# Optimization experiments

Measured on AMD Instinct MI355X. Metric: run time of the kernel, lower is better.

## Reference

```python
import jax, jax.numpy as jnp
import numpy as np

B, HH, WW, C = 2, 128, 128, 256
HEADS, KA, DR = 8, 3, 4
D = C // DR // HEADS          # 8 per-head channels
KK = KA * KA                  # 9 neighborhood positions
ATTN_DIM = KK * HEADS         # 72
DIMS = (ATTN_DIM // 4, ATTN_DIM // 2, ATTN_DIM)  # gnConv dims [18,36,72] (order=3)
SD = sum(DIMS)                # 126
S = 1.0                       # self.scale = s in __init__ (overrides qk scale)


def conv2d(x, w, b, pad, groups=1):
    out = jax.lax.conv_general_dilated(
        x, w, (1, 1), [(pad, pad), (pad, pad)],
        dimension_numbers=("NCHW", "OIHW", "NCHW"), feature_group_count=groups)
    return out + b[None, :, None, None]


def setup_inputs() -> dict:
    key = jax.random.key(0)
    ks = jax.random.split(key, 16)
    def rn(i, shape, s=0.02):
        return jax.random.normal(ks[i], shape, dtype=jnp.float32) * s
    return {
        "x": jax.random.normal(ks[0], (B, HH * WW, C), dtype=jnp.float32),
        "qkv_w": rn(1, (C, 3 * C // DR)),
        "qkv_b": jnp.zeros((3 * C // DR,), jnp.float32),
        "dc1_dw_w": rn(2, (D, 1, KA, KA)),
        "dc1_dw_b": jnp.zeros((D,), jnp.float32),
        "dc1_pw_w": rn(3, (KK * D, D, 3, 3)),
        "dc1_pw_b": jnp.zeros((KK * D,), jnp.float32),
        "dc2_dw_w": rn(4, (D, 1, KA, KA)),
        "dc2_dw_b": jnp.zeros((D,), jnp.float32),
        "dc2_pw_w": rn(5, (KK * D, D, 3, 3)),
        "dc2_pw_b": jnp.zeros((KK * D,), jnp.float32),
        "rpb": rn(6, (1, HEADS, 1, KK, 1, 1)),
        "pin_w": rn(7, (2 * ATTN_DIM, ATTN_DIM, 1, 1)),
        "pin_b": jnp.zeros((2 * ATTN_DIM,), jnp.float32),
        "dw7_w": rn(8, (SD, 1, 7, 7)),
        "dw7_b": jnp.zeros((SD,), jnp.float32),
        "dw5_w": rn(9, (SD, 1, 5, 5)),
        "dw5_b": jnp.zeros((SD,), jnp.float32),
        "dw3_w": rn(10, (SD, 1, 3, 3)),
        "dw3_b": jnp.zeros((SD,), jnp.float32),
        "pw1_w": rn(11, (DIMS[1], DIMS[0], 1, 1)),
        "pw1_b": jnp.zeros((DIMS[1],), jnp.float32),
        "pw2_w": rn(12, (DIMS[2], DIMS[1], 1, 1)),
        "pw2_b": jnp.zeros((DIMS[2],), jnp.float32),
        "pout_w": rn(13, (ATTN_DIM, ATTN_DIM, 1, 1)),
        "pout_b": jnp.zeros((ATTN_DIM,), jnp.float32),
        "proj_w": rn(14, (C // DR, C)),
        "proj_b": jnp.zeros((C,), jnp.float32),
        "H": HH,
        "W": WW,
    }


def reference(x, qkv_w, qkv_b, dc1_dw_w, dc1_dw_b, dc1_pw_w, dc1_pw_b,
              dc2_dw_w, dc2_dw_b, dc2_pw_w, dc2_pw_b, rpb, pin_w, pin_b,
              dw7_w, dw7_b, dw5_w, dw5_b, dw3_w, dw3_b,
              pw1_w, pw1_b, pw2_w, pw2_b, pout_w, pout_b, proj_w, proj_b, H, W):
    Bx, N, Cx = x.shape
    xi = x.reshape(Bx, H, W, Cx)
    qkv = xi @ qkv_w + qkv_b                                   # (B,H,W,3C/DR)
    f = jnp.transpose(qkv, (0, 3, 1, 2)).reshape(Bx * HEADS, 3 * D, H, W)
    q = (f[:, :D] * S).reshape(Bx, HEADS, D, 1, H, W)
    k_in = f[:, D:2 * D]                                       # (B*heads, D, H, W)
    v_in = f[:, 2 * D:]

    def dep(y):  # shared dep_conv + dep_conv1: KAxKA depthwise then 3x3 D->KK*D expand
        a = conv2d(conv2d(y, dc1_dw_w, dc1_dw_b, KA // 2, groups=D), dc1_pw_w, dc1_pw_b, 1)
        b2 = conv2d(conv2d(y, dc2_dw_w, dc2_dw_b, KA // 2, groups=D), dc2_pw_w, dc2_pw_b, 1)
        return (a + b2).reshape(Bx, HEADS, D, KK, H, W)

    k = dep(k_in) + rpb                                        # relative position bias
    v = dep(v_in)
    attn1 = jax.nn.softmax((q * k).sum(2, keepdims=True), axis=3)  # (B,heads,1,KK,H,W)

    # gnConv (recursive gated conv) on attention maps
    attn = attn1.reshape(Bx, HEADS * KK, H, W)                 # (B,72,H,W)
    fused = conv2d(attn, pin_w, pin_b, 0)                      # (B,144,H,W)
    pwa, abc = fused[:, :DIMS[0]], fused[:, DIMS[0]:]          # 18 / 126
    dw = conv2d(abc, dw7_w, dw7_b, 3, groups=SD)
    dw = conv2d(jax.nn.relu(dw), dw5_w, dw5_b, 2, groups=SD)
    dw = conv2d(jax.nn.relu(dw), dw3_w, dw3_b, 1, groups=SD) * S
    d0 = dw[:, :DIMS[0]]
    d1 = dw[:, DIMS[0]:DIMS[0] + DIMS[1]]
    d2 = dw[:, DIMS[0] + DIMS[1]:]
    g = pwa * d0
    g = conv2d(g, pw1_w, pw1_b, 0) * d1
    g = conv2d(g, pw2_w, pw2_b, 0) * d2
    g = conv2d(g, pout_w, pout_b, 0).reshape(Bx, HEADS, 1, KK, H, W)

    out = ((g * v) + (attn1 * v)).sum(3).reshape(Bx, Cx // DR, H, W)
    out = jnp.transpose(out, (0, 2, 3, 1)) @ proj_w + proj_b   # Linear C/DR -> C
    return out.reshape(Bx, N, Cx)
```

## Files before the change

### kernel.cpp

```cpp
#include <hip/hip_runtime.h>

#define IH 128
#define IW 128
#define NPI (IH*IW)

__global__ __launch_bounds__(256) void k_wt(const float* __restrict__ w1,
                                            const float* __restrict__ w2,
                                            float* __restrict__ wT) {
  int i = blockIdx.x * 256 + threadIdx.x;
  if (i < 72 * 72) {
    int c = i / 72, dkk = i % 72;
    wT[dkk * 144 + c]      = w1[i];
    wT[dkk * 144 + 72 + c] = w2[i];
  }
}

__global__ __launch_bounds__(256) void k_qkv(const float* __restrict__ x,
                                             const float* __restrict__ w,
                                             const float* __restrict__ bias,
                                             float* __restrict__ f) {
  int t = threadIdx.x;
  int lane = t & 63;
  int wv = __builtin_amdgcn_readfirstlane(t >> 6);
  int gp = blockIdx.x * 64 + lane;
  int b = gp >> 14;
  int pp = gp & (NPI - 1);
  const float* xrow = x + (size_t)gp * 256;
  int jbase = wv * 48;
  float acc[48];
#pragma unroll
  for (int jj = 0; jj < 48; ++jj) acc[jj] = bias[jbase + jj];
  for (int c = 0; c < 256; c += 8) {
    float xr[8];
#pragma unroll
    for (int q4 = 0; q4 < 2; ++q4) {
      float4 v = *reinterpret_cast<const float4*>(xrow + c + q4 * 4);
      xr[q4 * 4 + 0] = v.x; xr[q4 * 4 + 1] = v.y;
      xr[q4 * 4 + 2] = v.z; xr[q4 * 4 + 3] = v.w;
    }
#pragma unroll
    for (int jt = 0; jt < 48; jt += 4) {
#pragma unroll
      for (int cc = 0; cc < 8; ++cc) {
        const float* wp = w + (c + cc) * 192 + jbase + jt;
        acc[jt + 0] += xr[cc] * wp[0];
        acc[jt + 1] += xr[cc] * wp[1];
        acc[jt + 2] += xr[cc] * wp[2];
        acc[jt + 3] += xr[cc] * wp[3];
      }
    }
  }
#pragma unroll
  for (int jj = 0; jj < 48; ++jj) {
    int j = jbase + jj;
    f[((size_t)(b * 192 + j)) * NPI + pp] = acc[jj];
  }
}

template <int MODE>
__global__ __launch_bounds__(256) void k_dep(const float* __restrict__ f,
    const float* __restrict__ dwW1, const float* __restrict__ dwB1,
    const float* __restrict__ dwW2, const float* __restrict__ dwB2,
    const float* __restrict__ wT,  const float* __restrict__ pwB1,
    const float* __restrict__ pwB2, const float* __restrict__ rpb,
    const float* __restrict__ gout, const float* __restrict__ attn_in,
    float* __restrict__ outp) {
  __shared__ float kin[8][20][20];
  __shared__ float dwa[8][18][18];
  __shared__ float dwb[8][18][18];
  int t = threadIdx.x;
  int tile = blockIdx.x;
  int bh = blockIdx.y;
  int h = bh & 7;
  int y0 = (tile >> 3) << 4, x0 = (tile & 7) << 4;
  const float* src = f + ((size_t)(bh * 24 + (MODE ? 16 : 8))) * NPI;
  for (int idx = t; idx < 8 * 20 * 20; idx += 256) {
    int c = idx / 400, r = idx % 400, yy = r / 20, xx = r % 20;
    int ay = y0 - 2 + yy, ax = x0 - 2 + xx;
    float v = 0.f;
    if ((unsigned)ay < (unsigned)IH && (unsigned)ax < (unsigned)IW)
      v = src[c * NPI + ay * IW + ax];
    kin[c][yy][xx] = v;
  }
  __syncthreads();
  for (int idx = t; idx < 8 * 18 * 18; idx += 256) {
    int c = idx / 324, r = idx % 324, yy = r / 18, xx = r % 18;
    int ay = y0 - 1 + yy, ax = x0 - 1 + xx;
    float va = 0.f, vb = 0.f;
    if ((unsigned)ay < (unsigned)IH && (unsigned)ax < (unsigned)IW) {
      va = dwB1[c]; vb = dwB2[c];
#pragma unroll
      for (int ky = 0; ky < 3; ++ky)
#pragma unroll
        for (int kx = 0; kx < 3; ++kx) {
          float s = kin[c][yy + ky][xx + kx];
          va += dwW1[c * 9 + ky * 3 + kx] * s;
          vb += dwW2[c * 9 + ky * 3 + kx] * s;
        }
    }
    dwa[c][yy][xx] = va;
    dwb[c][yy][xx] = vb;
  }
  __syncthreads();
  int ly = t >> 4, lx = t & 15;
  int p = (y0 + ly) * IW + (x0 + lx);
  float acc[72];
#pragma unroll
  for (int c = 0; c < 72; ++c) {
    acc[c] = pwB1[c] + pwB2[c];
    if (MODE == 0) acc[c] += rpb[h * 9 + (c % 9)];
  }
#pragma unroll 1
  for (int dkk = 0; dkk < 72; ++dkk) {
    int d = dkk / 9; int t9 = dkk - d * 9; int ky = t9 / 3; int kx = t9 - ky * 3;
    float v1 = dwa[d][ly + ky][lx + kx];
    float v2 = dwb[d][ly + ky][lx + kx];
    const float* wp = wT + dkk * 144;
#pragma unroll
    for (int c = 0; c < 72; ++c) {
      acc[c] += wp[c] * v1;
      acc[c] += wp[72 + c] * v2;
    }
  }
  if (MODE == 0) {
    float q[8];
#pragma unroll
    for (int d = 0; d < 8; ++d) q[d] = f[((size_t)(bh * 24 + d)) * NPI + p];
    float e[9];
    float m = -1e30f;
#pragma unroll
    for (int kk = 0; kk < 9; ++kk) {
      float s = 0.f;
#pragma unroll
      for (int d = 0; d < 8; ++d) s += q[d] * acc[d * 9 + kk];
      e[kk] = s;
      m = fmaxf(m, s);
    }
    float sum = 0.f;
#pragma unroll
    for (int kk = 0; kk < 9; ++kk) { e[kk] = __expf(e[kk] - m); sum += e[kk]; }
    float r = 1.f / sum;
#pragma unroll
    for (int kk = 0; kk < 9; ++kk)
      outp[((size_t)(bh * 9 + kk)) * NPI + p] = e[kk] * r;
  } else {
    float coef[9];
#pragma unroll
    for (int kk = 0; kk < 9; ++kk)
      coef[kk] = gout[((size_t)(bh * 9 + kk)) * NPI + p] +
                 attn_in[((size_t)(bh * 9 + kk)) * NPI + p];
#pragma unroll
    for (int d = 0; d < 8; ++d) {
      float s = 0.f;
#pragma unroll
      for (int kk = 0; kk < 9; ++kk) s += coef[kk] * acc[d * 9 + kk];
      outp[((size_t)(bh * 8 + d)) * NPI + p] = s;
    }
  }
}

__global__ __launch_bounds__(256) void k_pin(const float* __restrict__ attn,
                                             const float* __restrict__ w,
                                             const float* __restrict__ bias,
                                             float* __restrict__ fused) {
  int t = threadIdx.x, lane = t & 63;
  int wv = __builtin_amdgcn_readfirstlane(t >> 6);
  int gp = blockIdx.x * 64 + lane;
  int b = gp >> 14, p = gp & (NPI - 1);
  const float* ap = attn + (size_t)b * 72 * NPI + p;
  float a[72];
#pragma unroll
  for (int i = 0; i < 72; ++i) a[i] = ap[i * NPI];
  int j0 = wv * 36;
#pragma unroll 1
  for (int jj = 0; jj < 36; ++jj) {
    int j = j0 + jj;
    const float* wp = w + j * 72;
    float s = bias[j];
#pragma unroll
    for (int i = 0; i < 72; ++i) s += wp[i] * a[i];
    fused[((size_t)b * 144 + j) * NPI + p] = s;
  }
}

__global__ __launch_bounds__(256) void k_dwchain(const float* __restrict__ fused,
    const float* __restrict__ w7, const float* __restrict__ b7,
    const float* __restrict__ w5, const float* __restrict__ b5,
    const float* __restrict__ w3, const float* __restrict__ b3,
    float* __restrict__ dwout) {
  __shared__ float s_in[28][28];
  __shared__ float s_t7[22][22];
  __shared__ float s_t5[18][18];
  int t = threadIdx.x;
  int tile = blockIdx.x;
  int c = blockIdx.y;
  int b = blockIdx.z;
  int y0 = (tile >> 3) << 4, x0 = (tile & 7) << 4;
  const float* src = fused + ((size_t)b * 144 + 18 + c) * NPI;
  for (int idx = t; idx < 28 * 28; idx += 256) {
    int yy = idx / 28, xx = idx % 28;
    int ay = y0 - 6 + yy, ax = x0 - 6 + xx;
    s_in[yy][xx] = ((unsigned)ay < (unsigned)IH && (unsigned)ax < (unsigned)IW)
                       ? src[ay * IW + ax] : 0.f;
  }
  __syncthreads();
  for (int idx = t; idx < 22 * 22; idx += 256) {
    int yy = idx / 22, xx = idx % 22;
    int ay = y0 - 3 + yy, ax = x0 - 3 + xx;
    float s = 0.f;
    if ((unsigned)ay < (unsigned)IH && (unsigned)ax < (unsigned)IW) {
      s = b7[c];
#pragma unroll
      for (int ky = 0; ky < 7; ++ky)
#pragma unroll
        for (int kx = 0; kx < 7; ++kx)
          s += w7[c * 49 + ky * 7 + kx] * s_in[yy + ky][xx + kx];
      s = fmaxf(s, 0.f);
    }
    s_t7[yy][xx] = s;
  }
  __syncthreads();
  for (int idx = t; idx < 18 * 18; idx += 256) {
    int yy = idx / 18, xx = idx % 18;
    int ay = y0 - 1 + yy, ax = x0 - 1 + xx;
    float s = 0.f;
    if ((unsigned)ay < (unsigned)IH && (unsigned)ax < (unsigned)IW) {
      s = b5[c];
#pragma unroll
      for (int ky = 0; ky < 5; ++ky)
#pragma unroll
        for (int kx = 0; kx < 5; ++kx)
          s += w5[c * 25 + ky * 5 + kx] * s_t7[yy + ky][xx + kx];
      s = fmaxf(s, 0.f);
    }
    s_t5[yy][xx] = s;
  }
  __syncthreads();
  int ly = t >> 4, lx = t & 15;
  float s = b3[c];
#pragma unroll
  for (int ky = 0; ky < 3; ++ky)
#pragma unroll
    for (int kx = 0; kx < 3; ++kx)
      s += w3[c * 9 + ky * 3 + kx] * s_t5[ly + ky][lx + kx];
  dwout[((size_t)b * 126 + c) * NPI + (y0 + ly) * IW + (x0 + lx)] = s;
}

__global__ __launch_bounds__(256) void k_g1(const float* __restrict__ fused,
                                            const float* __restrict__ dw,
                                            const float* __restrict__ w,
                                            const float* __restrict__ bias,
                                            float* __restrict__ g2) {
  int t = threadIdx.x, lane = t & 63;
  int wv = __builtin_amdgcn_readfirstlane(t >> 6);
  int gp = blockIdx.x * 64 + lane;
  int b = gp >> 14, p = gp & (NPI - 1);
  const float* fu = fused + (size_t)b * 144 * NPI + p;
  const float* dp = dw + (size_t)b * 126 * NPI + p;
  float g1v[18];
#pragma unroll
  for (int i = 0; i < 18; ++i) g1v[i] = fu[i * NPI] * dp[i * NPI];
  int j0 = wv * 9;
#pragma unroll 1
  for (int jj = 0; jj < 9; ++jj) {
    int j = j0 + jj;
    const float* wp = w + j * 18;
    float s = bias[j];
#pragma unroll
    for (int i = 0; i < 18; ++i) s += wp[i] * g1v[i];
    s *= dp[(18 + j) * NPI];
    g2[((size_t)b * 36 + j) * NPI + p] = s;
  }
}

__global__ __launch_bounds__(256) void k_g2(const float* __restrict__ g2in,
                                            const float* __restrict__ dw,
                                            const float* __restrict__ w,
                                            const float* __restrict__ bias,
                                            float* __restrict__ g3) {
  int t = threadIdx.x, lane = t & 63;
  int wv = __builtin_amdgcn_readfirstlane(t >> 6);
  int gp = blockIdx.x * 64 + lane;
  int b = gp >> 14, p = gp & (NPI - 1);
  const float* ip = g2in + (size_t)b * 36 * NPI + p;
  const float* dp = dw + (size_t)b * 126 * NPI + p;
  float g[36];
#pragma unroll
  for (int i = 0; i < 36; ++i) g[i] = ip[i * NPI];
  int j0 = wv * 18;
#pragma unroll 1
  for (int jj = 0; jj < 18; ++jj) {
    int j = j0 + jj;
    const float* wp = w + j * 36;
    float s = bias[j];
#pragma unroll
    for (int i = 0; i < 36; ++i) s += wp[i] * g[i];
    s *= dp[(54 + j) * NPI];
    g3[((size_t)b * 72 + j) * NPI + p] = s;
  }
}

__global__ __launch_bounds__(256) void k_g3(const float* __restrict__ g3in,
                                            const float* __restrict__ w,
                                            const float* __restrict__ bias,
                                            float* __restrict__ gout) {
  int t = threadIdx.x, lane = t & 63;
  int wv = __builtin_amdgcn_readfirstlane(t >> 6);
  int gp = blockIdx.x * 64 + lane;
  int b = gp >> 14, p = gp & (NPI - 1);
  const float* ip = g3in + (size_t)b * 72 * NPI + p;
  float g[72];
#pragma unroll
  for (int i = 0; i < 72; ++i) g[i] = ip[i * NPI];
  int j0 = wv * 18;
#pragma unroll 1
  for (int jj = 0; jj < 18; ++jj) {
    int j = j0 + jj;
    const float* wp = w + j * 72;
    float s = bias[j];
#pragma unroll
    for (int i = 0; i < 72; ++i) s += wp[i] * g[i];
    gout[((size_t)b * 72 + j) * NPI + p] = s;
  }
}

__global__ __launch_bounds__(256) void k_proj(const float* __restrict__ pre,
                                              const float* __restrict__ w,
                                              const float* __restrict__ bias,
                                              float* __restrict__ out) {
  int t = threadIdx.x;
  int blk = blockIdx.x;
  int b = (blk * 64) >> 14;
  int p0 = (blk * 64) & (NPI - 1);
  const float* pp = pre + (size_t)b * 64 * NPI + p0;
  float wreg[64];
#pragma unroll
  for (int i = 0; i < 64; ++i) wreg[i] = w[i * 256 + t];
  float bs = bias[t];
#pragma unroll 1
  for (int px = 0; px < 64; ++px) {
    float s = bs;
#pragma unroll
    for (int i = 0; i < 64; ++i) s += wreg[i] * pp[i * NPI + px];
    out[((size_t)(b * NPI + p0 + px)) * 256 + t] = s;
  }
}

extern "C" void kernel_launch(void* const* d_in, const int* in_sizes, int n_in,
                              void* d_out, int out_size, void* d_ws, size_t ws_size,
                              hipStream_t stream) {
  const float* x        = (const float*)d_in[0];
  const float* qkv_w    = (const float*)d_in[1];
  const float* qkv_b    = (const float*)d_in[2];
  const float* dc1_dw_w = (const float*)d_in[3];
  const float* dc1_dw_b = (const float*)d_in[4];
  const float* dc1_pw_w = (const float*)d_in[5];
  const float* dc1_pw_b = (const float*)d_in[6];
  const float* dc2_dw_w = (const float*)d_in[7];
  const float* dc2_dw_b = (const float*)d_in[8];
  const float* dc2_pw_w = (const float*)d_in[9];
  const float* dc2_pw_b = (const float*)d_in[10];
  const float* rpb      = (const float*)d_in[11];
  const float* pin_w    = (const float*)d_in[12];
  const float* pin_b    = (const float*)d_in[13];
  const float* dw7_w    = (const float*)d_in[14];
  const float* dw7_b    = (const float*)d_in[15];
  const float* dw5_w    = (const float*)d_in[16];
  const float* dw5_b    = (const float*)d_in[17];
  const float* dw3_w    = (const float*)d_in[18];
  const float* dw3_b    = (const float*)d_in[19];
  const float* pw1_w    = (const float*)d_in[20];
  const float* pw1_b    = (const float*)d_in[21];
  const float* pw2_w    = (const float*)d_in[22];
  const float* pw2_b    = (const float*)d_in[23];
  const float* pout_w   = (const float*)d_in[24];
  const float* pout_b   = (const float*)d_in[25];
  const float* proj_w   = (const float*)d_in[26];
  const float* proj_b   = (const float*)d_in[27];
  (void)in_sizes; (void)n_in; (void)out_size; (void)ws_size;

  float* fbuf = (float*)d_out;
  float* ws    = (float*)d_ws;
  float* wT    = ws;
  float* attn1 = wT + 10368;
  float* fused = attn1 + 2359296;
  float* dwout = fused + 4718592;
  float* g2b   = dwout + 4128768;
  float* g3b   = g2b + 1179648;
  float* goutb = g3b + 2359296;
  float* pre   = goutb + 2359296;

  hipLaunchKernelGGL(k_wt, dim3(21), dim3(256), 0, stream, dc1_pw_w, dc2_pw_w, wT);
  hipLaunchKernelGGL(k_qkv, dim3(512), dim3(256), 0, stream, x, qkv_w, qkv_b, fbuf);
  hipLaunchKernelGGL((k_dep<0>), dim3(64, 16), dim3(256), 0, stream, fbuf,
                     dc1_dw_w, dc1_dw_b, dc2_dw_w, dc2_dw_b, wT, dc1_pw_b, dc2_pw_b,
                     rpb, (const float*)nullptr, (const float*)nullptr, attn1);
  hipLaunchKernelGGL(k_pin, dim3(512), dim3(256), 0, stream, attn1, pin_w, pin_b, fused);
  hipLaunchKernelGGL(k_dwchain, dim3(64, 126, 2), dim3(256), 0, stream, fused,
                     dw7_w, dw7_b, dw5_w, dw5_b, dw3_w, dw3_b, dwout);
  hipLaunchKernelGGL(k_g1, dim3(512), dim3(256), 0, stream, fused, dwout, pw1_w, pw1_b, g2b);
  hipLaunchKernelGGL(k_g2, dim3(512), dim3(256), 0, stream, g2b, dwout, pw2_w, pw2_b, g3b);
  hipLaunchKernelGGL(k_g3, dim3(512), dim3(256), 0, stream, g3b, pout_w, pout_b, goutb);
  hipLaunchKernelGGL((k_dep<1>), dim3(64, 16), dim3(256), 0, stream, fbuf,
                     dc1_dw_w, dc1_dw_b, dc2_dw_w, dc2_dw_b, wT, dc1_pw_b, dc2_pw_b,
                     rpb, goutb, attn1, pre);
  hipLaunchKernelGGL(k_proj, dim3(512), dim3(256), 0, stream, pre, proj_w, proj_b,
                     (float*)d_out);
}
```

Measured before the change: 566.1 us.

## Fuse gnConv pointwise chain, stage qkv input in LDS, enlarge dwchain tiles

Merges the three gnConv pointwise kernels into one that keeps the 36- and 72-channel intermediates in shared memory, which removes two global round trips and two launches. The qkv kernel now stages the 64-pixel input tile in padded LDS so loads are coalesced. The depthwise chain uses 32x32 tiles to cut halo recompute. Other changes add launch_bounds occupancy hints, explicit FMAs, padded dep shared arrays, hoisted q/coef loads, and 4-pixel blocking in proj. The risks are register pressure from the occupancy hints and larger LDS footprints that may lower occupancy.

```diff
diff --git a/kernel.cpp b/kernel.cpp
--- a/kernel.cpp
+++ b/kernel.cpp
@@ -15,50 +15,50 @@
   }
 }
 
-__global__ __launch_bounds__(256) void k_qkv(const float* __restrict__ x,
-                                             const float* __restrict__ w,
-                                             const float* __restrict__ bias,
-                                             float* __restrict__ f) {
+__global__ __launch_bounds__(256, 4) void k_qkv(const float* __restrict__ x,
+                                                const float* __restrict__ w,
+                                                const float* __restrict__ bias,
+                                                float* __restrict__ f) {
+  __shared__ float xs[64][257];
   int t = threadIdx.x;
   int lane = t & 63;
-  int wv = __builtin_amdgcn_readfirstlane(t >> 6);
-  int gp = blockIdx.x * 64 + lane;
-  int b = gp >> 14;
-  int pp = gp & (NPI - 1);
-  const float* xrow = x + (size_t)gp * 256;
+  int wv = t >> 6;
+  int p0 = blockIdx.x * 64;
+  int b = p0 >> 14;
+  int pp = p0 & (NPI - 1);
+#pragma unroll
+  for (int k = 0; k < 16; ++k) {
+    int vi = k * 256 + t;
+    int px = vi >> 6;
+    int c = (vi & 63) * 4;
+    float4 v = *reinterpret_cast<const float4*>(x + (size_t)(p0 + px) * 256 + c);
+    xs[px][c] = v.x; xs[px][c + 1] = v.y; xs[px][c + 2] = v.z; xs[px][c + 3] = v.w;
+  }
+  __syncthreads();
   int jbase = wv * 48;
   float acc[48];
 #pragma unroll
   for (int jj = 0; jj < 48; ++jj) acc[jj] = bias[jbase + jj];
+#pragma unroll 1
   for (int c = 0; c < 256; c += 8) {
     float xr[8];
 #pragma unroll
-    for (int q4 = 0; q4 < 2; ++q4) {
-      float4 v = *reinterpret_cast<const float4*>(xrow + c + q4 * 4);
-      xr[q4 * 4 + 0] = v.x; xr[q4 * 4 + 1] = v.y;
-      xr[q4 * 4 + 2] = v.z; xr[q4 * 4 + 3] = v.w;
-    }
-#pragma unroll
-    for (int jt = 0; jt < 48; jt += 4) {
-#pragma unroll
-      for (int cc = 0; cc < 8; ++cc) {
-        const float* wp = w + (c + cc) * 192 + jbase + jt;
-        acc[jt + 0] += xr[cc] * wp[0];
-        acc[jt + 1] += xr[cc] * wp[1];
-        acc[jt + 2] += xr[cc] * wp[2];
-        acc[jt + 3] += xr[cc] * wp[3];
-      }
-    }
-  }
-#pragma unroll
-  for (int jj = 0; jj < 48; ++jj) {
-    int j = jbase + jj;
-    f[((size_t)(b * 192 + j)) * NPI + pp] = acc[jj];
-  }
+    for (int cc = 0; cc < 8; ++cc) xr[cc] = xs[lane][c + cc];
+#pragma unroll
+    for (int cc = 0; cc < 8; ++cc) {
+      const float* wp = w + (size_t)(c + cc) * 192 + jbase;
+#pragma unroll
+      for (int jj = 0; jj < 48; ++jj)
+        acc[jj] = __builtin_fmaf(xr[cc], wp[jj], acc[jj]);
+    }
+  }
+#pragma unroll
+  for (int jj = 0; jj < 48; ++jj)
+    f[((size_t)(b * 192 + jbase + jj)) * NPI + pp + lane] = acc[jj];
 }
 
 template <int MODE>
-__global__ __launch_bounds__(256) void k_dep(const float* __restrict__ f,
+__global__ __launch_bounds__(256, 4) void k_dep(const float* __restrict__ f,
     const float* __restrict__ dwW1, const float* __restrict__ dwB1,
     const float* __restrict__ dwW2, const float* __restrict__ dwB2,
     const float* __restrict__ wT,  const float* __restrict__ pwB1,
@@ -66,8 +66,8 @@
     const float* __restrict__ gout, const float* __restrict__ attn_in,
     float* __restrict__ outp) {
   __shared__ float kin[8][20][20];
-  __shared__ float dwa[8][18][18];
-  __shared__ float dwb[8][18][18];
+  __shared__ float dwa[8][18][20];
+  __shared__ float dwb[8][18][20];
   int t = threadIdx.x;
   int tile = blockIdx.x;
   int bh = blockIdx.y;
@@ -94,8 +94,8 @@
 #pragma unroll
         for (int kx = 0; kx < 3; ++kx) {
           float s = kin[c][yy + ky][xx + kx];
-          va += dwW1[c * 9 + ky * 3 + kx] * s;
-          vb += dwW2[c * 9 + ky * 3 + kx] * s;
+          va = __builtin_fmaf(dwW1[c * 9 + ky * 3 + kx], s, va);
+          vb = __builtin_fmaf(dwW2[c * 9 + ky * 3 + kx], s, vb);
         }
     }
     dwa[c][yy][xx] = va;
@@ -110,29 +110,39 @@
     acc[c] = pwB1[c] + pwB2[c];
     if (MODE == 0) acc[c] += rpb[h * 9 + (c % 9)];
   }
+  float q[8]; float coef[9];
+  if (MODE == 0) {
+#pragma unroll
+    for (int d = 0; d < 8; ++d) q[d] = f[((size_t)(bh * 24 + d)) * NPI + p];
+  } else {
+#pragma unroll
+    for (int kk = 0; kk < 9; ++kk)
+      coef[kk] = gout[((size_t)(bh * 9 + kk)) * NPI + p] +
+                 attn_in[((size_t)(bh * 9 + kk)) * NPI + p];
+  }
 #pragma unroll 1
-  for (int dkk = 0; dkk < 72; ++dkk) {
-    int d = dkk / 9; int t9 = dkk - d * 9; int ky = t9 / 3; int kx = t9 - ky * 3;
-    float v1 = dwa[d][ly + ky][lx + kx];
-    float v2 = dwb[d][ly + ky][lx + kx];
-    const float* wp = wT + dkk * 144;
-#pragma unroll
-    for (int c = 0; c < 72; ++c) {
-      acc[c] += wp[c] * v1;
-      acc[c] += wp[72 + c] * v2;
+  for (int d = 0; d < 8; ++d) {
+#pragma unroll
+    for (int t9 = 0; t9 < 9; ++t9) {
+      const int ky = t9 / 3, kx = t9 % 3;
+      const float v1 = dwa[d][ly + ky][lx + kx];
+      const float v2 = dwb[d][ly + ky][lx + kx];
+      const float* wp = wT + (size_t)(d * 9 + t9) * 144;
+#pragma unroll
+      for (int c = 0; c < 72; ++c) {
+        acc[c] = __builtin_fmaf(wp[c], v1, acc[c]);
+        acc[c] = __builtin_fmaf(wp[72 + c], v2, acc[c]);
+      }
     }
   }
   if (MODE == 0) {
-    float q[8];
-#pragma unroll
-    for (int d = 0; d < 8; ++d) q[d] = f[((size_t)(bh * 24 + d)) * NPI + p];
     float e[9];
     float m = -1e30f;
 #pragma unroll
     for (int kk = 0; kk < 9; ++kk) {
       float s = 0.f;
 #pragma unroll
-      for (int d = 0; d < 8; ++d) s += q[d] * acc[d * 9 + kk];
+      for (int d = 0; d < 8; ++d) s = __builtin_fmaf(q[d], acc[d * 9 + kk], s);
       e[kk] = s;
       m = fmaxf(m, s);
     }
@@ -144,27 +154,22 @@
     for (int kk = 0; kk < 9; ++kk)
       outp[((size_t)(bh * 9 + kk)) * NPI + p] = e[kk] * r;
   } else {
-    float coef[9];
-#pragma unroll
-    for (int kk = 0; kk < 9; ++kk)
-      coef[kk] = gout[((size_t)(bh * 9 + kk)) * NPI + p] +
-                 attn_in[((size_t)(bh * 9 + kk)) * NPI + p];
 #pragma unroll
     for (int d = 0; d < 8; ++d) {
       float s = 0.f;
 #pragma unroll
-      for (int kk = 0; kk < 9; ++kk) s += coef[kk] * acc[d * 9 + kk];
+      for (int kk = 0; kk < 9; ++kk) s = __builtin_fmaf(coef[kk], acc[d * 9 + kk], s);
       outp[((size_t)(bh * 8 + d)) * NPI + p] = s;
     }
   }
 }
 
-__global__ __launch_bounds__(256) void k_pin(const float* __restrict__ attn,
-                                             const float* __restrict__ w,
-                                             const float* __restrict__ bias,
-                                             float* __restrict__ fused) {
+__global__ __launch_bounds__(256, 4) void k_pin(const float* __restrict__ attn,
+                                                const float* __restrict__ w,
+                                                const float* __restrict__ bias,
+                                                float* __restrict__ fused) {
   int t = threadIdx.x, lane = t & 63;
-  int wv = __builtin_amdgcn_readfirstlane(t >> 6);
+  int wv = t >> 6;
   int gp = blockIdx.x * 64 + lane;
   int b = gp >> 14, p = gp & (NPI - 1);
   const float* ap = attn + (size_t)b * 72 * NPI + p;
@@ -172,40 +177,40 @@
 #pragma unroll
   for (int i = 0; i < 72; ++i) a[i] = ap[i * NPI];
   int j0 = wv * 36;
-#pragma unroll 1
+#pragma unroll 2
   for (int jj = 0; jj < 36; ++jj) {
     int j = j0 + jj;
     const float* wp = w + j * 72;
     float s = bias[j];
 #pragma unroll
-    for (int i = 0; i < 72; ++i) s += wp[i] * a[i];
+    for (int i = 0; i < 72; ++i) s = __builtin_fmaf(wp[i], a[i], s);
     fused[((size_t)b * 144 + j) * NPI + p] = s;
   }
 }
 
-__global__ __launch_bounds__(256) void k_dwchain(const float* __restrict__ fused,
+__global__ __launch_bounds__(256, 4) void k_dwchain(const float* __restrict__ fused,
     const float* __restrict__ w7, const float* __restrict__ b7,
     const float* __restrict__ w5, const float* __restrict__ b5,
     const float* __restrict__ w3, const float* __restrict__ b3,
     float* __restrict__ dwout) {
-  __shared__ float s_in[28][28];
-  __shared__ float s_t7[22][22];
-  __shared__ float s_t5[18][18];
+  __shared__ float s_in[44][44];
+  __shared__ float s_t7[38][38];
+  __shared__ float s_t5[34][34];
   int t = threadIdx.x;
   int tile = blockIdx.x;
   int c = blockIdx.y;
   int b = blockIdx.z;
-  int y0 = (tile >> 3) << 4, x0 = (tile & 7) << 4;
+  int y0 = (tile >> 2) << 5, x0 = (tile & 3) << 5;
   const float* src = fused + ((size_t)b * 144 + 18 + c) * NPI;
-  for (int idx = t; idx < 28 * 28; idx += 256) {
-    int yy = idx / 28, xx = idx % 28;
+  for (int idx = t; idx < 44 * 44; idx += 256) {
+    int yy = idx / 44, xx = idx % 44;
     int ay = y0 - 6 + yy, ax = x0 - 6 + xx;
     s_in[yy][xx] = ((unsigned)ay < (unsigned)IH && (unsigned)ax < (unsigned)IW)
                        ? src[ay * IW + ax] : 0.f;
   }
   __syncthreads();
-  for (int idx = t; idx < 22 * 22; idx += 256) {
-    int yy = idx / 22, xx = idx % 22;
+  for (int idx = t; idx < 38 * 38; idx += 256) {
+    int yy = idx / 38, xx = idx % 38;
     int ay = y0 - 3 + yy, ax = x0 - 3 + xx;
     float s = 0.f;
     if ((unsigned)ay < (unsigned)IH && (unsigned)ax < (unsigned)IW) {
@@ -214,14 +219,14 @@
       for (int ky = 0; ky < 7; ++ky)
 #pragma unroll
         for (int kx = 0; kx < 7; ++kx)
-          s += w7[c * 49 + ky * 7 + kx] * s_in[yy + ky][xx + kx];
+          s = __builtin_fmaf(w7[c * 49 + ky * 7 + kx], s_in[yy + ky][xx + kx], s);
       s = fmaxf(s, 0.f);
     }
     s_t7[yy][xx] = s;
   }
   __syncthreads();
-  for (int idx = t; idx < 18 * 18; idx += 256) {
-    int yy = idx / 18, xx = idx % 18;
+  for (int idx = t; idx < 34 * 34; idx += 256) {
+    int yy = idx / 34, xx = idx % 34;
     int ay = y0 - 1 + yy, ax = x0 - 1 + xx;
     float s = 0.f;
     if ((unsigned)ay < (unsigned)IH && (unsigned)ax < (unsigned)IW) {
@@ -230,29 +235,34 @@
       for (int ky = 0; ky < 5; ++ky)
 #pragma unroll
         for (int kx = 0; kx < 5; ++kx)
-          s += w5[c * 25 + ky * 5 + kx] * s_t7[yy + ky][xx + kx];
+          s = __builtin_fmaf(w5[c * 25 + ky * 5 + kx], s_t7[yy + ky][xx + kx], s);
       s = fmaxf(s, 0.f);
     }
     s_t5[yy][xx] = s;
   }
   __syncthreads();
-  int ly = t >> 4, lx = t & 15;
-  float s = b3[c];
-#pragma unroll
-  for (int ky = 0; ky < 3; ++ky)
-#pragma unroll
-    for (int kx = 0; kx < 3; ++kx)
-      s += w3[c * 9 + ky * 3 + kx] * s_t5[ly + ky][lx + kx];
-  dwout[((size_t)b * 126 + c) * NPI + (y0 + ly) * IW + (x0 + lx)] = s;
-}
-
-__global__ __launch_bounds__(256) void k_g1(const float* __restrict__ fused,
-                                            const float* __restrict__ dw,
-                                            const float* __restrict__ w,
-                                            const float* __restrict__ bias,
-                                            float* __restrict__ g2) {
+  for (int idx = t; idx < 32 * 32; idx += 256) {
+    int py = idx >> 5, px = idx & 31;
+    float s = b3[c];
+#pragma unroll
+    for (int ky = 0; ky < 3; ++ky)
+#pragma unroll
+      for (int kx = 0; kx < 3; ++kx)
+        s = __builtin_fmaf(w3[c * 9 + ky * 3 + kx], s_t5[py + ky][px + kx], s);
+    dwout[((size_t)b * 126 + c) * NPI + (y0 + py) * IW + (x0 + px)] = s;
+  }
+}
+
+__global__ __launch_bounds__(256, 4) void k_gchain(const float* __restrict__ fused,
+    const float* __restrict__ dw,
+    const float* __restrict__ pw1_w, const float* __restrict__ pw1_b,
+    const float* __restrict__ pw2_w, const float* __restrict__ pw2_b,
+    const float* __restrict__ pout_w, const float* __restrict__ pout_b,
+    float* __restrict__ gout) {
+  __shared__ float t36[36][64];
+  __shared__ float t72[72][64];
   int t = threadIdx.x, lane = t & 63;
-  int wv = __builtin_amdgcn_readfirstlane(t >> 6);
+  int wv = t >> 6;
   int gp = blockIdx.x * 64 + lane;
   int b = gp >> 14, p = gp & (NPI - 1);
   const float* fu = fused + (size_t)b * 144 * NPI + p;
@@ -260,74 +270,58 @@
   float g1v[18];
 #pragma unroll
   for (int i = 0; i < 18; ++i) g1v[i] = fu[i * NPI] * dp[i * NPI];
-  int j0 = wv * 9;
-#pragma unroll 1
-  for (int jj = 0; jj < 9; ++jj) {
-    int j = j0 + jj;
-    const float* wp = w + j * 18;
-    float s = bias[j];
-#pragma unroll
-    for (int i = 0; i < 18; ++i) s += wp[i] * g1v[i];
-    s *= dp[(18 + j) * NPI];
-    g2[((size_t)b * 36 + j) * NPI + p] = s;
-  }
-}
-
-__global__ __launch_bounds__(256) void k_g2(const float* __restrict__ g2in,
-                                            const float* __restrict__ dw,
-                                            const float* __restrict__ w,
-                                            const float* __restrict__ bias,
-                                            float* __restrict__ g3) {
-  int t = threadIdx.x, lane = t & 63;
-  int wv = __builtin_amdgcn_readfirstlane(t >> 6);
-  int gp = blockIdx.x * 64 + lane;
-  int b = gp >> 14, p = gp & (NPI - 1);
-  const float* ip = g2in + (size_t)b * 36 * NPI + p;
-  const float* dp = dw + (size_t)b * 126 * NPI + p;
-  float g[36];
-#pragma unroll
-  for (int i = 0; i < 36; ++i) g[i] = ip[i * NPI];
-  int j0 = wv * 18;
-#pragma unroll 1
-  for (int jj = 0; jj < 18; ++jj) {
-    int j = j0 + jj;
-    const float* wp = w + j * 36;
-    float s = bias[j];
-#pragma unroll
-    for (int i = 0; i < 36; ++i) s += wp[i] * g[i];
-    s *= dp[(54 + j) * NPI];
-    g3[((size_t)b * 72 + j) * NPI + p] = s;
-  }
-}
-
-__global__ __launch_bounds__(256) void k_g3(const float* __restrict__ g3in,
-                                            const float* __restrict__ w,
-                                            const float* __restrict__ bias,
-                                            float* __restrict__ gout) {
-  int t = threadIdx.x, lane = t & 63;
-  int wv = __builtin_amdgcn_readfirstlane(t >> 6);
-  int gp = blockIdx.x * 64 + lane;
-  int b = gp >> 14, p = gp & (NPI - 1);
-  const float* ip = g3in + (size_t)b * 72 * NPI + p;
-  float g[72];
-#pragma unroll
-  for (int i = 0; i < 72; ++i) g[i] = ip[i * NPI];
-  int j0 = wv * 18;
-#pragma unroll 1
-  for (int jj = 0; jj < 18; ++jj) {
-    int j = j0 + jj;
-    const float* wp = w + j * 72;
-    float s = bias[j];
-#pragma unroll
-    for (int i = 0; i < 72; ++i) s += wp[i] * g[i];
-    gout[((size_t)b * 72 + j) * NPI + p] = s;
-  }
-}
-
-__global__ __launch_bounds__(256) void k_proj(const float* __restrict__ pre,
-                                              const float* __restrict__ w,
-                                              const float* __restrict__ bias,
-                                              float* __restrict__ out) {
+  {
+    int j0 = wv * 9;
+#pragma unroll 2
+    for (int jj = 0; jj < 9; ++jj) {
+      int j = j0 + jj;
+      const float* wp = pw1_w + j * 18;
+      float s = pw1_b[j];
+#pragma unroll
+      for (int i = 0; i < 18; ++i) s = __builtin_fmaf(wp[i], g1v[i], s);
+      s *= dp[(18 + j) * NPI];
+      t36[j][lane] = s;
+    }
+  }
+  __syncthreads();
+  {
+    float a36[36];
+#pragma unroll
+    for (int i = 0; i < 36; ++i) a36[i] = t36[i][lane];
+    int j0 = wv * 18;
+#pragma unroll 2
+    for (int jj = 0; jj < 18; ++jj) {
+      int j = j0 + jj;
+      const float* wp = pw2_w + j * 36;
+      float s = pw2_b[j];
+#pragma unroll
+      for (int i = 0; i < 36; ++i) s = __builtin_fmaf(wp[i], a36[i], s);
+      s *= dp[(54 + j) * NPI];
+      t72[j][lane] = s;
+    }
+  }
+  __syncthreads();
+  {
+    float a72[72];
+#pragma unroll
+    for (int i = 0; i < 72; ++i) a72[i] = t72[i][lane];
+    int j0 = wv * 18;
+#pragma unroll 2
+    for (int jj = 0; jj < 18; ++jj) {
+      int j = j0 + jj;
+      const float* wp = pout_w + j * 72;
+      float s = pout_b[j];
+#pragma unroll
+      for (int i = 0; i < 72; ++i) s = __builtin_fmaf(wp[i], a72[i], s);
+      gout[((size_t)b * 72 + j) * NPI + p] = s;
+    }
+  }
+}
+
+__global__ __launch_bounds__(256, 4) void k_proj(const float* __restrict__ pre,
+                                                 const float* __restrict__ w,
+                                                 const float* __restrict__ bias,
+                                                 float* __restrict__ out) {
   int t = threadIdx.x;
   int blk = blockIdx.x;
   int b = (blk * 64) >> 14;
@@ -338,11 +332,18 @@
   for (int i = 0; i < 64; ++i) wreg[i] = w[i * 256 + t];
   float bs = bias[t];
 #pragma unroll 1
-  for (int px = 0; px < 64; ++px) {
-    float s = bs;
-#pragma unroll
-    for (int i = 0; i < 64; ++i) s += wreg[i] * pp[i * NPI + px];
-    out[((size_t)(b * NPI + p0 + px)) * 256 + t] = s;
+  for (int px4 = 0; px4 < 16; ++px4) {
+    float s0 = bs, s1 = bs, s2 = bs, s3 = bs;
+#pragma unroll
+    for (int i = 0; i < 64; ++i) {
+      const float* rp = pp + (size_t)i * NPI + px4 * 4;
+      s0 = __builtin_fmaf(wreg[i], rp[0], s0);
+      s1 = __builtin_fmaf(wreg[i], rp[1], s1);
+      s2 = __builtin_fmaf(wreg[i], rp[2], s2);
+      s3 = __builtin_fmaf(wreg[i], rp[3], s3);
+    }
+    size_t ob = ((size_t)(b * NPI + p0 + px4 * 4)) * 256 + t;
+    out[ob] = s0; out[ob + 256] = s1; out[ob + 512] = s2; out[ob + 768] = s3;
   }
 }
 
@@ -385,9 +386,7 @@
   float* attn1 = wT + 10368;
   float* fused = attn1 + 2359296;
   float* dwout = fused + 4718592;
-  float* g2b   = dwout + 4128768;
-  float* g3b   = g2b + 1179648;
-  float* goutb = g3b + 2359296;
+  float* goutb = dwout + 4128768;
   float* pre   = goutb + 2359296;
 
   hipLaunchKernelGGL(k_wt, dim3(21), dim3(256), 0, stream, dc1_pw_w, dc2_pw_w, wT);
@@ -396,11 +395,10 @@
                      dc1_dw_w, dc1_dw_b, dc2_dw_w, dc2_dw_b, wT, dc1_pw_b, dc2_pw_b,
                      rpb, (const float*)nullptr, (const float*)nullptr, attn1);
   hipLaunchKernelGGL(k_pin, dim3(512), dim3(256), 0, stream, attn1, pin_w, pin_b, fused);
-  hipLaunchKernelGGL(k_dwchain, dim3(64, 126, 2), dim3(256), 0, stream, fused,
+  hipLaunchKernelGGL(k_dwchain, dim3(16, 126, 2), dim3(256), 0, stream, fused,
                      dw7_w, dw7_b, dw5_w, dw5_b, dw3_w, dw3_b, dwout);
-  hipLaunchKernelGGL(k_g1, dim3(512), dim3(256), 0, stream, fused, dwout, pw1_w, pw1_b, g2b);
-  hipLaunchKernelGGL(k_g2, dim3(512), dim3(256), 0, stream, g2b, dwout, pw2_w, pw2_b, g3b);
-  hipLaunchKernelGGL(k_g3, dim3(512), dim3(256), 0, stream, g3b, pout_w, pout_b, goutb);
+  hipLaunchKernelGGL(k_gchain, dim3(512), dim3(256), 0, stream, fused, dwout,
+                     pw1_w, pw1_b, pw2_w, pw2_b, pout_w, pout_b, goutb);
   hipLaunchKernelGGL((k_dep<1>), dim3(64, 16), dim3(256), 0, stream, fbuf,
                      dc1_dw_w, dc1_dw_b, dc2_dw_w, dc2_dw_b, wT, dc1_pw_b, dc2_pw_b,
                      rpb, goutb, attn1, pre);
```

Result: slower. 925.2 us (+63.5%).
